# Kernel optimization log

Hardware: AMD Instinct MI355X
Metric: run time of the kernel (lower is better)

The kernel has to match this reference:

```python
import jax, jax.numpy as jnp
import numpy as np

BSZ, SEQ, DIM = 2, 2048, 4096
N_HEADS, N_KV_HEADS, HEAD_DIM = 32, 8, 128
N_REP = N_HEADS // N_KV_HEADS
MAX_BS, MAX_SEQ = 4, 2048
ROPE_THETA = 500000.0


def setup_inputs() -> dict:
    key = jax.random.key(0)
    ks = jax.random.split(key, 6)
    sc = 1.0 / np.sqrt(DIM)
    x = jax.random.normal(ks[0], (BSZ, SEQ, DIM), jnp.float32)
    wq = jax.random.normal(ks[1], (DIM, N_HEADS * HEAD_DIM), jnp.float32) * sc
    wk = jax.random.normal(ks[2], (DIM, N_KV_HEADS * HEAD_DIM), jnp.float32) * sc
    wv = jax.random.normal(ks[3], (DIM, N_KV_HEADS * HEAD_DIM), jnp.float32) * sc
    wo = jax.random.normal(ks[4], (N_HEADS * HEAD_DIM, DIM), jnp.float32) * sc
    cache_k = jnp.zeros((MAX_BS, MAX_SEQ, N_KV_HEADS, HEAD_DIM), jnp.float32)
    cache_v = jnp.zeros((MAX_BS, MAX_SEQ, N_KV_HEADS, HEAD_DIM), jnp.float32)
    # precomputed rotary frequencies (freqs_cis = cos + i*sin)
    inv = 1.0 / (ROPE_THETA ** (np.arange(0, HEAD_DIM, 2, dtype=np.float32) / HEAD_DIM))
    t = np.arange(SEQ, dtype=np.float32)
    freqs = np.outer(t, inv)  # [SEQ, HEAD_DIM//2]
    freqs_cos = jnp.asarray(np.cos(freqs), jnp.float32)
    freqs_sin = jnp.asarray(np.sin(freqs), jnp.float32)
    # causal additive mask, broadcast over (batch, heads)
    neg = jnp.full((SEQ, SEQ), -1e9, jnp.float32)
    mask = jnp.triu(neg, k=1)[None, None, :, :]
    return {"x": x, "wq": wq, "wk": wk, "wv": wv, "wo": wo,
            "cache_k": cache_k, "cache_v": cache_v,
            "freqs_cos": freqs_cos, "freqs_sin": freqs_sin,
            "mask": mask, "start_pos": 0}


def _apply_rope(t, cos, sin):
    # t: [b, s, h, d]; complex multiply on (even, odd) pairs
    b, s, h, d = t.shape
    tr = t.reshape(b, s, h, d // 2, 2)
    a, bb = tr[..., 0], tr[..., 1]
    cos = cos[None, :, None, :]
    sin = sin[None, :, None, :]
    out = jnp.stack([a * cos - bb * sin, a * sin + bb * cos], axis=-1)
    return out.reshape(b, s, h, d)


def reference(x, wq, wk, wv, wo, cache_k, cache_v, freqs_cos, freqs_sin, mask, start_pos):
    bsz, seqlen, _ = x.shape
    xq = (x @ wq).reshape(bsz, seqlen, N_HEADS, HEAD_DIM)
    xk = (x @ wk).reshape(bsz, seqlen, N_KV_HEADS, HEAD_DIM)
    xv = (x @ wv).reshape(bsz, seqlen, N_KV_HEADS, HEAD_DIM)
    xq = _apply_rope(xq, freqs_cos, freqs_sin)
    xk = _apply_rope(xk, freqs_cos, freqs_sin)
    # KV-cache append (start_pos is a static Python int)
    cache_k = jax.lax.dynamic_update_slice(cache_k, xk, (0, start_pos, 0, 0))
    cache_v = jax.lax.dynamic_update_slice(cache_v, xv, (0, start_pos, 0, 0))
    keys = cache_k[:bsz, : start_pos + seqlen]    # [b, kv_len, kvh, d]
    values = cache_v[:bsz, : start_pos + seqlen]
    # GQA repeat_kv: tile kv heads n_rep times -> [b, kv_len, H, d]
    keys = jnp.repeat(keys, N_REP, axis=2)
    values = jnp.repeat(values, N_REP, axis=2)
    q = xq.transpose(0, 2, 1, 3)        # [b, H, s, d]
    k = keys.transpose(0, 2, 1, 3)      # [b, H, kv, d]
    v = values.transpose(0, 2, 1, 3)
    scores = jnp.einsum('bhqd,bhkd->bhqk', q, k) / np.sqrt(HEAD_DIM)
    if mask is not None:
        scores = scores + mask
    probs = jax.nn.softmax(scores.astype(jnp.float32), axis=-1).astype(q.dtype)
    out = jnp.einsum('bhqk,bhkd->bhqd', probs, v)
    out = out.transpose(0, 2, 1, 3).reshape(bsz, seqlen, -1)
    return out @ wo
```

## Files before the change

### kernel.cpp

```cpp
#include <hip/hip_runtime.h>
#include <hip/hip_bf16.h>
#include <cstdint>

typedef __attribute__((ext_vector_type(8))) __bf16 bf16x8;
typedef __attribute__((ext_vector_type(4))) __bf16 bf16x4;
typedef __attribute__((ext_vector_type(2))) __bf16 bf16x2;
typedef __attribute__((ext_vector_type(4))) float  f32x4;

#define MFMA16(a,b,c) __builtin_amdgcn_mfma_f32_16x16x32_bf16((a),(b),(c),0,0,0)

__device__ __forceinline__ void gl16(const void* g, void* l) {
  __builtin_amdgcn_global_load_lds(
      (const __attribute__((address_space(1))) void*)g,
      (__attribute__((address_space(3))) void*)l, 16, 0, 0);
}

static constexpr int BSZ = 2, SEQ = 2048, DIM = 4096;
static constexpr int NH = 32, NKV = 8, HD = 128;
static constexpr int TOK = BSZ * SEQ;
static constexpr int NQKV = NH*HD + 2*NKV*HD;
static constexpr float QSCALE = 0.08838834764831845f;
static constexpr float FNEG = -3.0e38f;

__global__ __launch_bounds__(256) void f32_to_bf16_k(const float* __restrict__ in,
                                                     __bf16* __restrict__ out) {
  int i = (blockIdx.x * 256 + threadIdx.x) * 4;
  float4 v = *(const float4*)(in + i);
  bf16x4 o = { (__bf16)v.x, (__bf16)v.y, (__bf16)v.z, (__bf16)v.w };
  *(bf16x4*)(out + i) = o;
}

__global__ __launch_bounds__(256) void wtrans64_k(const float* __restrict__ S,
                                                  __bf16* __restrict__ D, int sC) {
  __shared__ __align__(16) __bf16 t[64 * 66];
  const int tid = threadIdx.x;
  const int cb = blockIdx.x, rb = blockIdx.y;
#pragma unroll
  for (int i = 0; i < 16; ++i) {
    int e = i * 256 + tid; int r = e >> 6, c = e & 63;
    t[c * 66 + r] = (__bf16)S[(size_t)(rb * 64 + r) * sC + cb * 64 + c];
  }
  __syncthreads();
#pragma unroll
  for (int i = 0; i < 16; ++i) {
    int e = i * 256 + tid; int c = e >> 6, r = e & 63;
    D[(size_t)(cb * 64 + c) * 4096 + rb * 64 + r] = t[c * 66 + r];
  }
}

__global__ __launch_bounds__(256) void gemm_bf16_bt_k(const __bf16* __restrict__ A,
                                                      const __bf16* __restrict__ Bt,
                                                      float* __restrict__ C,
                                                      int M, int N, int K) {
  __shared__ __align__(16) __bf16 lA[128 * 64];
  __shared__ __align__(16) __bf16 lB[128 * 64];
  const int tid = threadIdx.x, lane = tid & 63, wid = tid >> 6;
  const int bm = blockIdx.y, bn = blockIdx.x;
  const int wm = wid & 1, wn = wid >> 1;
  f32x4 acc[4][4] = {};

  const int srow = lane >> 3, scol = lane & 7;
  const __bf16* Ag = A + ((size_t)bm * 128 + wid * 8 + srow) * K + scol * 8;
  const __bf16* Bg = Bt + ((size_t)bn * 128 + wid * 8 + srow) * K + scol * 8;
  __bf16* lAw = lA + wid * 512;
  __bf16* lBw = lB + wid * 512;

  const int nk = K >> 6;
  for (int kt = 0; kt < nk; ++kt) {
    const __bf16* ag = Ag + (size_t)kt * 64;
    const __bf16* bg = Bg + (size_t)kt * 64;
#pragma unroll
    for (int i = 0; i < 4; ++i) {
      gl16(ag + (size_t)i * 32 * K, lAw + i * 2048);
      gl16(bg + (size_t)i * 32 * K, lBw + i * 2048);
    }
    __syncthreads();
#pragma unroll
    for (int kk = 0; kk < 2; ++kk) {
      bf16x8 af[4], bfv[4];
#pragma unroll
      for (int m = 0; m < 4; ++m)
        af[m] = *(const bf16x8*)&lA[(wm * 64 + m * 16 + (lane & 15)) * 64 + kk * 32 + (lane >> 4) * 8];
#pragma unroll
      for (int n = 0; n < 4; ++n)
        bfv[n] = *(const bf16x8*)&lB[(wn * 64 + n * 16 + (lane & 15)) * 64 + kk * 32 + (lane >> 4) * 8];
#pragma unroll
      for (int m = 0; m < 4; ++m)
#pragma unroll
        for (int n = 0; n < 4; ++n)
          acc[m][n] = MFMA16(af[m], bfv[n], acc[m][n]);
    }
    __syncthreads();
  }
  const int r0 = (lane >> 4) * 4, cN = lane & 15;
#pragma unroll
  for (int m = 0; m < 4; ++m) {
    size_t row = (size_t)bm * 128 + wm * 64 + m * 16 + r0;
#pragma unroll
    for (int n = 0; n < 4; ++n) {
      size_t col = (size_t)bn * 128 + wn * 64 + n * 16 + cN;
#pragma unroll
      for (int r = 0; r < 4; ++r)
        C[(row + r) * N + col] = acc[m][n][r];
    }
  }
}

__global__ __launch_bounds__(256) void rope_qk_k(const float* __restrict__ QKV,
                                                 const float* __restrict__ fc,
                                                 const float* __restrict__ fs,
                                                 __bf16* __restrict__ Qb,
                                                 __bf16* __restrict__ Kb) {
  int idx = blockIdx.x * 256 + threadIdx.x;
  int tok = idx / 2560;
  int rem = idx - tok * 2560;
  int head = rem >> 6, p = rem & 63;
  int b = tok >> 11, s = tok & 2047;
  float2 v = *(const float2*)(QKV + (size_t)tok * NQKV + head * 128 + 2 * p);
  float c = fc[s * 64 + p], sn = fs[s * 64 + p];
  float x = v.x * c - v.y * sn;
  float y = v.x * sn + v.y * c;
  if (head < 32) {
    x *= QSCALE; y *= QSCALE;
    bf16x2 o = { (__bf16)x, (__bf16)y };
    *(bf16x2*)(Qb + ((size_t)(b * 32 + head) * 2048 + s) * 128 + 2 * p) = o;
  } else {
    bf16x2 o = { (__bf16)x, (__bf16)y };
    *(bf16x2*)(Kb + ((size_t)(b * 8 + head - 32) * 2048 + s) * 128 + 2 * p) = o;
  }
}

__global__ __launch_bounds__(256) void vtrans_k(const float* __restrict__ QKV,
                                                __bf16* __restrict__ Vt) {
  __shared__ __align__(16) __bf16 t[128 * 66];
  const int sb = blockIdx.x, hk = blockIdx.y, b = blockIdx.z;
  const int tid = threadIdx.x;
#pragma unroll
  for (int i = 0; i < 32; ++i) {
    int e = i * 256 + tid; int s = e >> 7, d = e & 127;
    t[d * 66 + s] = (__bf16)QKV[(size_t)(b * 2048 + sb * 64 + s) * NQKV + 5120 + hk * 128 + d];
  }
  __syncthreads();
  int d = tid >> 1, s0 = (tid & 1) * 32;
  __bf16* dst = Vt + ((size_t)(b * 8 + hk) * 128 + d) * 2048 + sb * 64 + s0;
  const unsigned* srcu = (const unsigned*)&t[d * 66 + s0];
  unsigned* dstu = (unsigned*)dst;
#pragma unroll
  for (int i = 0; i < 16; ++i) dstu[i] = srcu[i];
}

__global__ __launch_bounds__(256, 2) void attn128_k(const __bf16* __restrict__ Q,
                                                    const __bf16* __restrict__ Kc,
                                                    const __bf16* __restrict__ Vt,
                                                    __bf16* __restrict__ Ab) {
  __shared__ __align__(16) __bf16 lK[2][64 * 128];
  __shared__ __align__(16) __bf16 lV[2][128 * 64];
  __shared__ __align__(16) __bf16 lP[4][16 * 64];
  const int qt = gridDim.x - 1 - blockIdx.x;
  const int h = blockIdx.y, b = blockIdx.z;
  const int hk = h >> 2;
  const int tid = threadIdx.x, lane = tid & 63, wid = tid >> 6;
  const int qb = qt * 128;
  const int lo = lane & 15, hi = lane >> 4;
  const int xk = (lo & 7) * 8;
  const int srow8 = lane >> 3, scol8 = lane & 7;
  const __bf16* Qp = Q + ((size_t)(b * 32 + h) * 2048 + qb) * 128;
  const __bf16* Kp = Kc + (size_t)(b * 8 + hk) * 2048 * 128;
  const __bf16* Vp = Vt + (size_t)(b * 8 + hk) * 128 * 2048;

  bf16x8 qf[2][4];
#pragma unroll
  for (int rt = 0; rt < 2; ++rt)
#pragma unroll
    for (int kq = 0; kq < 4; ++kq)
      qf[rt][kq] = *(const bf16x8*)(Qp + (size_t)(rt * 64 + wid * 16 + lo) * 128 + kq * 32 + hi * 8);

  f32x4 accO[2][8] = {};
  float mr[2][4] = { { FNEG, FNEG, FNEG, FNEG }, { FNEG, FNEG, FNEG, FNEG } };
  float lr[2][4] = {};

  const int nkb = 2 * qt + 2;

  auto STAGE = [&](int t) {
    const int kbase = t * 64;
    __bf16* dK = lK[t & 1];
    __bf16* dV = lV[t & 1];
#pragma unroll
    for (int i = 0; i < 4; ++i) {
      const int krow = (i * 4 + wid) * 4 + hi;
      gl16(Kp + (size_t)(kbase + krow) * 128 + (lo ^ (krow & 7)) * 8,
           dK + (i * 4 + wid) * 512);
      const int vrow = (i * 4 + wid) * 8 + srow8;
      gl16(Vp + (size_t)vrow * 2048 + kbase + (scol8 ^ srow8) * 8,
           dV + (i * 4 + wid) * 512);
    }
  };

  STAGE(0);
  asm volatile("s_waitcnt vmcnt(0)" ::: "memory");
  __builtin_amdgcn_s_barrier();

  for (int kb = 0; kb < nkb; ++kb) {
    const int cur = kb & 1;
    if (kb + 1 < nkb) STAGE(kb + 1);
    const bool maskb = (kb >= nkb - 2);
    const __bf16* bK = lK[cur];
    const __bf16* bV = lV[cur];

#pragma unroll
    for (int rt = 0; rt < 2; ++rt) {
      f32x4 sc[4] = {};
      __builtin_amdgcn_s_setprio(1);
#pragma unroll
      for (int nb = 0; nb < 4; ++nb)
#pragma unroll
        for (int kk = 0; kk < 4; ++kk) {
          bf16x8 kf = *(const bf16x8*)&bK[(nb * 16 + lo) * 128 + ((kk * 32 + hi * 8) ^ xk)];
          sc[nb] = MFMA16(qf[rt][kk], kf, sc[nb]);
        }
      __builtin_amdgcn_s_setprio(0);

      const int qrow0 = qb + rt * 64 + wid * 16 + hi * 4;
      const int kcol0 = kb * 64 + lo;
      float tm[4] = { FNEG, FNEG, FNEG, FNEG };
#pragma unroll
      for (int nb = 0; nb < 4; ++nb)
#pragma unroll
        for (int r = 0; r < 4; ++r) {
          float s = sc[nb][r];
          if (maskb && (kcol0 + nb * 16 > qrow0 + r)) s = FNEG;
          sc[nb][r] = s;
          tm[r] = fmaxf(tm[r], s);
        }
#pragma unroll
      for (int r = 0; r < 4; ++r) {
#pragma unroll
        for (int off = 1; off < 16; off <<= 1)
          tm[r] = fmaxf(tm[r], __shfl_xor(tm[r], off));
        float mn = fmaxf(mr[rt][r], tm[r]);
        tm[r] = __expf(mr[rt][r] - mn);
        mr[rt][r] = mn;
      }
      float rs[4] = {};
#pragma unroll
      for (int nb = 0; nb < 4; ++nb)
#pragma unroll
        for (int r = 0; r < 4; ++r) {
          float p = __expf(sc[nb][r] - mr[rt][r]);
          rs[r] += p;
          const int q = hi * 4 + r;
          lP[wid][q * 64 + ((nb * 16 + lo) ^ ((q & 7) * 8))] = (__bf16)p;
        }
#pragma unroll
      for (int r = 0; r < 4; ++r) {
#pragma unroll
        for (int off = 1; off < 16; off <<= 1)
          rs[r] += __shfl_xor(rs[r], off);
        lr[rt][r] = lr[rt][r] * tm[r] + rs[r];
      }
#pragma unroll
      for (int nb2 = 0; nb2 < 8; ++nb2)
#pragma unroll
        for (int r = 0; r < 4; ++r)
          accO[rt][nb2][r] *= tm[r];

      __builtin_amdgcn_s_setprio(1);
#pragma unroll
      for (int kk = 0; kk < 2; ++kk) {
        bf16x8 pf = *(const bf16x8*)&lP[wid][lo * 64 + ((kk * 32 + hi * 8) ^ xk)];
#pragma unroll
        for (int nb2 = 0; nb2 < 8; ++nb2) {
          bf16x8 vf = *(const bf16x8*)&bV[(nb2 * 16 + lo) * 64 + ((kk * 32 + hi * 8) ^ xk)];
          accO[rt][nb2] = MFMA16(pf, vf, accO[rt][nb2]);
        }
      }
      __builtin_amdgcn_s_setprio(0);
    }

    if (kb + 1 < nkb) asm volatile("s_waitcnt vmcnt(0)" ::: "memory");
    __builtin_amdgcn_s_barrier();
  }

#pragma unroll
  for (int rt = 0; rt < 2; ++rt) {
    float inv[4];
#pragma unroll
    for (int r = 0; r < 4; ++r) inv[r] = 1.0f / lr[rt][r];
#pragma unroll
    for (int nb2 = 0; nb2 < 8; ++nb2)
#pragma unroll
      for (int r = 0; r < 4; ++r)
        Ab[((size_t)b * 2048 + qb + rt * 64 + wid * 16 + hi * 4 + r) * 4096 + h * 128 + nb2 * 16 + lo] =
            (__bf16)(accO[rt][nb2][r] * inv[r]);
  }
}

extern "C" void kernel_launch(void* const* d_in, const int* in_sizes, int n_in,
                              void* d_out, int out_size, void* d_ws, size_t ws_size,
                              hipStream_t stream) {
  const float* x  = (const float*)d_in[0];
  const float* wq = (const float*)d_in[1];
  const float* wk = (const float*)d_in[2];
  const float* wv = (const float*)d_in[3];
  const float* wo = (const float*)d_in[4];
  const float* fc = (const float*)d_in[7];
  const float* fs = (const float*)d_in[8];
  float* out = (float*)d_out;

  char* ws = (char*)d_ws;
  __bf16* Wqkvt = (__bf16*)(ws + 0);
  __bf16* Wot   = (__bf16*)(ws + 50331648);
  __bf16* Qb    = (__bf16*)(ws + 83886080);
  __bf16* Kb    = (__bf16*)(ws + 117440512);
  __bf16* Vtb   = (__bf16*)(ws + 125829120);
  __bf16* Xbf   = (__bf16*)(ws + 134217728);
  float*  QKVf  = (float*)(ws + 167772160);
  __bf16* Ab    = (__bf16*)(ws + 167772160);

  f32_to_bf16_k<<<TOK * DIM / 1024, 256, 0, stream>>>(x, Xbf);
  wtrans64_k<<<dim3(64, 64), 256, 0, stream>>>(wq, Wqkvt, 4096);
  wtrans64_k<<<dim3(16, 64), 256, 0, stream>>>(wk, Wqkvt + (size_t)4096 * 4096, 1024);
  wtrans64_k<<<dim3(16, 64), 256, 0, stream>>>(wv, Wqkvt + (size_t)5120 * 4096, 1024);
  wtrans64_k<<<dim3(64, 64), 256, 0, stream>>>(wo, Wot, 4096);

  gemm_bf16_bt_k<<<dim3(48, 32), 256, 0, stream>>>(Xbf, Wqkvt, QKVf, TOK, NQKV, DIM);

  rope_qk_k<<<TOK * 40 * 64 / 256, 256, 0, stream>>>(QKVf, fc, fs, Qb, Kb);
  vtrans_k<<<dim3(32, 8, 2), 256, 0, stream>>>(QKVf, Vtb);

  attn128_k<<<dim3(16, 32, 2), 256, 0, stream>>>(Qb, Kb, Vtb, Ab);

  gemm_bf16_bt_k<<<dim3(32, 32), 256, 0, stream>>>(Ab, Wot, out, TOK, DIM, DIM);
}
```

Measured before the change: 1.124 ms.

## Double-buffer GEMM LDS tiles with block swizzle and compile-time shapes

Replaces the single-buffered bf16 GEMM with a templated kernel that prefetches the next K tile into a second LDS buffer while the current one is consumed. This removes one barrier per iteration and overlaps global loads with MFMA work. It also remaps the 1D block index with an XCD-style swizzle so that neighbouring tiles share operand reuse in cache, and raises the MFMA wave priority around the compute block. The cost is doubled LDS use (64KB per block) under a launch bound of 2 blocks per CU, which may limit occupancy.

```diff
diff --git a/kernel.cpp b/kernel.cpp
--- a/kernel.cpp
+++ b/kernel.cpp
@@ -48,51 +48,67 @@
   }
 }
 
-__global__ __launch_bounds__(256) void gemm_bf16_bt_k(const __bf16* __restrict__ A,
-                                                      const __bf16* __restrict__ Bt,
-                                                      float* __restrict__ C,
-                                                      int M, int N, int K) {
-  __shared__ __align__(16) __bf16 lA[128 * 64];
-  __shared__ __align__(16) __bf16 lB[128 * 64];
+template<int M, int N, int K>
+__global__ __launch_bounds__(256, 2) void gemm2p_k(const __bf16* __restrict__ A,
+                                                   const __bf16* __restrict__ Bt,
+                                                   float* __restrict__ C) {
+  __shared__ __align__(16) __bf16 lA[2][128 * 64];
+  __shared__ __align__(16) __bf16 lB[2][128 * 64];
+  constexpr int NBX = N / 128;
+  constexpr int NWG = (M / 128) * NBX;
+  const int lin = blockIdx.x;
+  const int swz = (lin & 7) * (NWG / 8) + (lin >> 3);
+  const int bm = swz / NBX, bn = swz % NBX;
   const int tid = threadIdx.x, lane = tid & 63, wid = tid >> 6;
-  const int bm = blockIdx.y, bn = blockIdx.x;
   const int wm = wid & 1, wn = wid >> 1;
+  const int lo = lane & 15, hi = lane >> 4;
   f32x4 acc[4][4] = {};
 
   const int srow = lane >> 3, scol = lane & 7;
   const __bf16* Ag = A + ((size_t)bm * 128 + wid * 8 + srow) * K + scol * 8;
   const __bf16* Bg = Bt + ((size_t)bn * 128 + wid * 8 + srow) * K + scol * 8;
-  __bf16* lAw = lA + wid * 512;
-  __bf16* lBw = lB + wid * 512;
-
-  const int nk = K >> 6;
-  for (int kt = 0; kt < nk; ++kt) {
+
+  auto STAGE = [&](int kt) {
+    __bf16* dA = lA[kt & 1] + wid * 512;
+    __bf16* dB = lB[kt & 1] + wid * 512;
     const __bf16* ag = Ag + (size_t)kt * 64;
     const __bf16* bg = Bg + (size_t)kt * 64;
 #pragma unroll
     for (int i = 0; i < 4; ++i) {
-      gl16(ag + (size_t)i * 32 * K, lAw + i * 2048);
-      gl16(bg + (size_t)i * 32 * K, lBw + i * 2048);
-    }
-    __syncthreads();
+      gl16(ag + (size_t)i * 32 * K, dA + i * 2048);
+      gl16(bg + (size_t)i * 32 * K, dB + i * 2048);
+    }
+  };
+
+  constexpr int NK = K / 64;
+  STAGE(0);
+  __syncthreads();
+
+  for (int kt = 0; kt < NK; ++kt) {
+    if (kt + 1 < NK) STAGE(kt + 1);
+    const __bf16* bA = lA[kt & 1];
+    const __bf16* bB = lB[kt & 1];
 #pragma unroll
     for (int kk = 0; kk < 2; ++kk) {
       bf16x8 af[4], bfv[4];
 #pragma unroll
       for (int m = 0; m < 4; ++m)
-        af[m] = *(const bf16x8*)&lA[(wm * 64 + m * 16 + (lane & 15)) * 64 + kk * 32 + (lane >> 4) * 8];
+        af[m] = *(const bf16x8*)&bA[(wm * 64 + m * 16 + lo) * 64 + kk * 32 + hi * 8];
 #pragma unroll
       for (int n = 0; n < 4; ++n)
-        bfv[n] = *(const bf16x8*)&lB[(wn * 64 + n * 16 + (lane & 15)) * 64 + kk * 32 + (lane >> 4) * 8];
+        bfv[n] = *(const bf16x8*)&bB[(wn * 64 + n * 16 + lo) * 64 + kk * 32 + hi * 8];
+      __builtin_amdgcn_s_setprio(1);
 #pragma unroll
       for (int m = 0; m < 4; ++m)
 #pragma unroll
         for (int n = 0; n < 4; ++n)
           acc[m][n] = MFMA16(af[m], bfv[n], acc[m][n]);
+      __builtin_amdgcn_s_setprio(0);
     }
     __syncthreads();
   }
-  const int r0 = (lane >> 4) * 4, cN = lane & 15;
+
+  const int r0 = hi * 4, cN = lo;
 #pragma unroll
   for (int m = 0; m < 4; ++m) {
     size_t row = (size_t)bm * 128 + wm * 64 + m * 16 + r0;
@@ -323,12 +339,12 @@
   wtrans64_k<<<dim3(16, 64), 256, 0, stream>>>(wv, Wqkvt + (size_t)5120 * 4096, 1024);
   wtrans64_k<<<dim3(64, 64), 256, 0, stream>>>(wo, Wot, 4096);
 
-  gemm_bf16_bt_k<<<dim3(48, 32), 256, 0, stream>>>(Xbf, Wqkvt, QKVf, TOK, NQKV, DIM);
+  gemm2p_k<4096, 6144, 4096><<<1536, 256, 0, stream>>>(Xbf, Wqkvt, QKVf);
 
   rope_qk_k<<<TOK * 40 * 64 / 256, 256, 0, stream>>>(QKVf, fc, fs, Qb, Kb);
   vtrans_k<<<dim3(32, 8, 2), 256, 0, stream>>>(QKVf, Vtb);
 
   attn128_k<<<dim3(16, 32, 2), 256, 0, stream>>>(Qb, Kb, Vtb, Ab);
 
-  gemm_bf16_bt_k<<<dim3(32, 32), 256, 0, stream>>>(Ab, Wot, out, TOK, DIM, DIM);
-}
+  gemm2p_k<4096, 4096, 4096><<<1024, 256, 0, stream>>>(Ab, Wot, out);
+}
```

Result: no change. 1.106 ms (-1.6%).
